# Performance work log

Measured on AMD Instinct MI355X. Metric: run time of the kernel, lower is better.

## Reference

```python
import jax, jax.numpy as jnp
import numpy as np

B, N, D_IN, D_OUT = 2, 2048, 2048, 2048
H, G = 16, 4            # num_heads, n_kv_groups
HD = D_OUT // H         # head_dim = 128
REP = H // G            # query heads per kv head = 4


def setup_inputs() -> dict:
    key = jax.random.key(0)
    ks = jax.random.split(key, 6)
    s = lambda fan_in: 1.0 / np.sqrt(fan_in)
    return {
        "x": jax.random.normal(ks[0], (B, N, D_IN), jnp.float32),
        "Wq": jax.random.normal(ks[1], (D_IN, D_OUT), jnp.float32) * s(D_IN),
        "Wk": jax.random.normal(ks[2], (D_IN, G * HD), jnp.float32) * s(D_IN),
        "Wv": jax.random.normal(ks[3], (D_IN, G * HD), jnp.float32) * s(D_IN),
        "Wo": jax.random.normal(ks[4], (D_OUT, D_OUT), jnp.float32) * s(D_OUT),
        "bo": jnp.zeros((D_OUT,), jnp.float32),
    }


def reference(x, Wq, Wk, Wv, Wo, bo):
    b, n, _ = x.shape
    # projections
    q = (x @ Wq).reshape(b, n, G, REP, HD)   # query heads grouped: h = g*REP + r
    k = (x @ Wk).reshape(b, n, G, HD)
    v = (x @ Wv).reshape(b, n, G, HD)
    # grouped attention scores; KV broadcast over REP instead of repeat_kv
    scores = jnp.einsum('bqgrd,bkgd->bgrqk', q, k)  # [b,G,REP,N,N]
    causal = jnp.tril(jnp.ones((n, n), bool))       # allowed positions
    scores = jnp.where(causal, scores, -jnp.inf)
    w = jax.nn.softmax(scores / np.float32(np.sqrt(HD)), axis=-1)
    ctx = jnp.einsum('bgrqk,bkgd->bqgrd', w, v).reshape(b, n, D_OUT)
    return ctx @ Wo + bo
```

## Files before the change

### kernel.cpp

```cpp
#include <hip/hip_runtime.h>
#include <stdint.h>

typedef __attribute__((ext_vector_type(8))) __bf16 bf16x8;
typedef __attribute__((ext_vector_type(4))) float f32x4;
typedef __attribute__((ext_vector_type(4))) short short4v;

static constexpr int SEQ  = 2048;
static constexpr int DQKV = 3072;
static constexpr int HD   = 128;

__device__ __forceinline__ short f2bf(float f) {
  unsigned u = __builtin_bit_cast(unsigned, f);
  u += 0x7fffu + ((u >> 16) & 1u);
  return (short)(u >> 16);
}

__device__ __forceinline__ unsigned pack2(float a, float b) {
  return (unsigned)(unsigned short)f2bf(a) | ((unsigned)(unsigned short)f2bf(b) << 16);
}

__device__ __forceinline__ void gl_lds16(const void* g, void* l) {
  __builtin_amdgcn_global_load_lds(
      (const __attribute__((address_space(1))) void*)g,
      (__attribute__((address_space(3))) void*)l, 16, 0, 0);
}

__global__ __launch_bounds__(256) void cast_x_kernel(const float* __restrict__ x,
                                                     short* __restrict__ xb) {
  int i = blockIdx.x * 256 + threadIdx.x;
  float4 v = reinterpret_cast<const float4*>(x)[i];
  short4v o;
  o[0] = f2bf(v.x); o[1] = f2bf(v.y); o[2] = f2bf(v.z); o[3] = f2bf(v.w);
  *reinterpret_cast<short4v*>(xb + (size_t)i * 4) = o;
}

__global__ __launch_bounds__(256) void tcast_w_kernel(const float* __restrict__ in,
                                                      short* __restrict__ out,
                                                      int R, int C) {
  __shared__ float tile[32][33];
  int c0 = blockIdx.x * 32, r0 = blockIdx.y * 32;
  int tx = threadIdx.x, ty = threadIdx.y;
  for (int i = 0; i < 4; i++)
    tile[ty + i * 8][tx] = in[(size_t)(r0 + ty + i * 8) * C + c0 + tx];
  __syncthreads();
  for (int i = 0; i < 4; i++)
    out[(size_t)(c0 + ty + i * 8) * R + r0 + tx] = f2bf(tile[tx][ty + i * 8]);
}

__global__ __launch_bounds__(256) void transpose_v_kernel(const short* __restrict__ qkv,
                                                          short* __restrict__ vT) {
  __shared__ short tile[32][33];
  int n0 = blockIdx.x * 32, c0 = blockIdx.y * 32, b = blockIdx.z;
  int tx = threadIdx.x, ty = threadIdx.y;
  for (int i = 0; i < 4; i++)
    tile[ty + i * 8][tx] = qkv[(size_t)(b * SEQ + n0 + ty + i * 8) * DQKV + 2560 + c0 + tx];
  __syncthreads();
  for (int i = 0; i < 4; i++)
    vT[(size_t)(b * 512 + c0 + ty + i * 8) * SEQ + n0 + tx] = tile[tx][ty + i * 8];
}

template <int F32OUT>
__global__ __launch_bounds__(256)
void gemm_bt_kernel(const short* __restrict__ A, const short* __restrict__ BT,
                    void* __restrict__ Cout, const float* __restrict__ bias,
                    int M, int N, int K, int qcols, float qscale) {
  __shared__ __align__(16) short As[4096];
  __shared__ __align__(16) short Bs[4096];
  const int tid = threadIdx.x, lane = tid & 63, w = tid >> 6;
  const int l15 = lane & 15, quad = lane >> 4, q8 = quad * 8;
  const int row0 = blockIdx.y * 128, col0 = blockIdx.x * 128;
  const int wm = (w >> 1) * 64, wn = (w & 1) * 64;
  f32x4 acc[4][4] = {};
  const short* ga0 = A  + (size_t)(row0 + w * 16 + (lane >> 2)) * K + (lane & 3) * 8;
  const short* gb0 = BT + (size_t)(col0 + w * 16 + (lane >> 2)) * K + (lane & 3) * 8;
  for (int kt = 0; kt < K; kt += 32) {
    gl_lds16(ga0 + kt,                   As + w * 512);
    gl_lds16(ga0 + (size_t)64 * K + kt,  As + 2048 + w * 512);
    gl_lds16(gb0 + kt,                   Bs + w * 512);
    gl_lds16(gb0 + (size_t)64 * K + kt,  Bs + 2048 + w * 512);
    __syncthreads();
    bf16x8 af[4], bfr[4];
    for (int i = 0; i < 4; i++)
      af[i] = *reinterpret_cast<const bf16x8*>(As + (wm + i * 16 + l15) * 32 + q8);
    for (int j = 0; j < 4; j++)
      bfr[j] = *reinterpret_cast<const bf16x8*>(Bs + (wn + j * 16 + l15) * 32 + q8);
    for (int i = 0; i < 4; i++)
      for (int j = 0; j < 4; j++)
        acc[i][j] = __builtin_amdgcn_mfma_f32_16x16x32_bf16(af[i], bfr[j], acc[i][j], 0, 0, 0);
    __syncthreads();
  }
  if (F32OUT) {
    float* C = (float*)Cout;
    for (int j = 0; j < 4; j++) {
      int col = col0 + wn + j * 16 + l15;
      float bv = bias[col];
      for (int i = 0; i < 4; i++)
        for (int r = 0; r < 4; r++)
          C[(size_t)(row0 + wm + i * 16 + quad * 4 + r) * N + col] = acc[i][j][r] + bv;
    }
  } else {
    short* C = (short*)Cout;
    for (int j = 0; j < 4; j++) {
      int col = col0 + wn + j * 16 + l15;
      float sc = (col < qcols) ? qscale : 1.0f;
      for (int i = 0; i < 4; i++)
        for (int r = 0; r < 4; r++)
          C[(size_t)(row0 + wm + i * 16 + quad * 4 + r) * N + col] = f2bf(acc[i][j][r] * sc);
    }
  }
}

__global__ __launch_bounds__(256)
void attn_kernel(const short* __restrict__ qkv, const short* __restrict__ vT,
                 short* __restrict__ ctx) {
  __shared__ __align__(16) short Ks[8192];
  __shared__ __align__(16) short Vs[8192];
  __shared__ __align__(16) short Ps[4608];
  const int tid = threadIdx.x, lane = tid & 63, w = tid >> 6;
  const int l15 = lane & 15, quad = lane >> 4, q8 = quad * 8;
  const int idx = blockIdx.x;
  const int qt = 31 - (idx >> 5);
  const int h = (idx >> 1) & 15, b = idx & 1, g = h >> 2;

  bf16x8 qf[4];
  {
    const short* gq = qkv + (size_t)(b * SEQ + qt * 64 + w * 16 + l15) * DQKV + h * HD + q8;
    for (int ds = 0; ds < 4; ds++)
      qf[ds] = *reinterpret_cast<const bf16x8*>(gq + ds * 32);
  }
  bf16x8 ones;
  for (int i = 0; i < 8; i++) ones[i] = __builtin_bit_cast(__bf16, (short)0x3F80);

  f32x4 acco[8] = {};
  f32x4 accl = {};

  for (int kt = 0; kt <= qt; kt++) {
    __syncthreads();
    {
      const short* gk = qkv + (size_t)(b * SEQ + kt * 64 + w * 16 + (lane >> 2)) * DQKV +
                        2048 + g * HD + (lane & 3) * 8;
      for (int ks = 0; ks < 4; ks++)
        gl_lds16(gk + ks * 32, Ks + ks * 2048 + w * 512);
      for (int c = 0; c < 2; c++)
        for (int ih = 0; ih < 2; ih++)
          gl_lds16(vT + (size_t)(b * 512 + g * HD + ih * 64 + w * 16 + (lane >> 2)) * SEQ +
                       kt * 64 + c * 32 + (lane & 3) * 8,
                   Vs + c * 4096 + ih * 2048 + w * 512);
    }
    __syncthreads();

    f32x4 accs[4] = {};
    for (int ds = 0; ds < 4; ds++)
      for (int j = 0; j < 4; j++) {
        bf16x8 kf = *reinterpret_cast<const bf16x8*>(Ks + ds * 2048 + (j * 16 + l15) * 32 + q8);
        accs[j] = __builtin_amdgcn_mfma_f32_16x16x32_bf16(kf, qf[ds], accs[j], 0, 0, 0);
      }

    if (kt == qt) {
      const int q = w * 16 + l15;
      for (int j = 0; j < 4; j++)
        for (int r = 0; r < 4; r++)
          if (j * 16 + quad * 4 + r > q) accs[j][r] = -1e38f;
    }

    for (int j = 0; j < 4; j++) {
      float p0 = exp2f(accs[j][0]), p1 = exp2f(accs[j][1]);
      float p2 = exp2f(accs[j][2]), p3 = exp2f(accs[j][3]);
      unsigned u0 = __builtin_bit_cast(unsigned, p0), u1 = __builtin_bit_cast(unsigned, p1);
      unsigned u2 = __builtin_bit_cast(unsigned, p2), u3 = __builtin_bit_cast(unsigned, p3);
      uint2 dd = make_uint2((u0 >> 16) | (u1 & 0xffff0000u),
                            (u2 >> 16) | (u3 & 0xffff0000u));
      *reinterpret_cast<uint2*>(Ps + w * 1152 + l15 * 72 + j * 16 + quad * 4) = dd;
    }
    asm volatile("s_waitcnt lgkmcnt(0)" ::: "memory");

    for (int c = 0; c < 2; c++) {
      bf16x8 pf = *reinterpret_cast<const bf16x8*>(Ps + w * 1152 + l15 * 72 + c * 32 + q8);
      accl = __builtin_amdgcn_mfma_f32_16x16x32_bf16(ones, pf, accl, 0, 0, 0);
      for (int nt = 0; nt < 8; nt++) {
        bf16x8 vf = *reinterpret_cast<const bf16x8*>(Vs + c * 4096 + (nt * 16 + l15) * 32 + q8);
        acco[nt] = __builtin_amdgcn_mfma_f32_16x16x32_bf16(vf, pf, acco[nt], 0, 0, 0);
      }
    }
  }

  const float invl = 1.f / accl[0];
  const size_t row = (size_t)(b * SEQ + qt * 64 + w * 16 + l15);
  for (int nt = 0; nt < 8; nt++) {
    uint2 dd = make_uint2(pack2(acco[nt][0] * invl, acco[nt][1] * invl),
                          pack2(acco[nt][2] * invl, acco[nt][3] * invl));
    *reinterpret_cast<uint2*>(ctx + row * 2048 + h * HD + nt * 16 + quad * 4) = dd;
  }
}

extern "C" void kernel_launch(void* const* d_in, const int* in_sizes, int n_in,
                              void* d_out, int out_size, void* d_ws, size_t ws_size,
                              hipStream_t stream) {
  const float* x  = (const float*)d_in[0];
  const float* Wq = (const float*)d_in[1];
  const float* Wk = (const float*)d_in[2];
  const float* Wv = (const float*)d_in[3];
  const float* Wo = (const float*)d_in[4];
  const float* bo = (const float*)d_in[5];
  float* out = (float*)d_out;

  const float sc2 = 0.08838834764831845f * 1.4426950408889634f;

  short* xb    = (short*)d_ws;
  short* WqkvT = xb    + (size_t)4096 * 2048;
  short* WoT   = WqkvT + (size_t)3072 * 2048;
  short* qkv   = WoT   + (size_t)2048 * 2048;
  short* vT    = qkv   + (size_t)4096 * 3072;
  short* ctx   = vT    + (size_t)1024 * 2048;

  cast_x_kernel<<<dim3(8192), dim3(256), 0, stream>>>(x, xb);
  tcast_w_kernel<<<dim3(64, 64), dim3(32, 8), 0, stream>>>(Wq, WqkvT, 2048, 2048);
  tcast_w_kernel<<<dim3(16, 64), dim3(32, 8), 0, stream>>>(Wk, WqkvT + (size_t)2048 * 2048, 2048, 512);
  tcast_w_kernel<<<dim3(16, 64), dim3(32, 8), 0, stream>>>(Wv, WqkvT + (size_t)2560 * 2048, 2048, 512);
  tcast_w_kernel<<<dim3(64, 64), dim3(32, 8), 0, stream>>>(Wo, WoT, 2048, 2048);

  gemm_bt_kernel<0><<<dim3(24, 32), dim3(256), 0, stream>>>(xb, WqkvT, qkv, nullptr,
                                                            4096, 3072, 2048, 2048, sc2);
  transpose_v_kernel<<<dim3(64, 16, 2), dim3(32, 8), 0, stream>>>(qkv, vT);
  attn_kernel<<<dim3(1024), dim3(256), 0, stream>>>(qkv, vT, ctx);
  gemm_bt_kernel<1><<<dim3(16, 32), dim3(256), 0, stream>>>(ctx, WoT, out, bo,
                                                            4096, 2048, 2048, 0, 1.0f);
}
```

Before: 325.3 us.

## Fuse prep kernels, fold V transpose into QKV GEMM, double-buffer attention K/V

Merges the x cast and four weight transpose-casts into a single launch, and writes the transposed V directly from the QKV GEMM epilogue, removing the separate transpose kernel. GEMM blocks use a swizzled 1D grid to group tiles for cache locality. The attention kernel double-buffers K/V tiles in LDS so the next tile's loads overlap compute, at the cost of doubled LDS use per block.

```diff
diff --git a/kernel.cpp b/kernel.cpp
--- a/kernel.cpp
+++ b/kernel.cpp
@@ -25,21 +25,30 @@
       (__attribute__((address_space(3))) void*)l, 16, 0, 0);
 }
 
-__global__ __launch_bounds__(256) void cast_x_kernel(const float* __restrict__ x,
-                                                     short* __restrict__ xb) {
-  int i = blockIdx.x * 256 + threadIdx.x;
-  float4 v = reinterpret_cast<const float4*>(x)[i];
-  short4v o;
-  o[0] = f2bf(v.x); o[1] = f2bf(v.y); o[2] = f2bf(v.z); o[3] = f2bf(v.w);
-  *reinterpret_cast<short4v*>(xb + (size_t)i * 4) = o;
-}
-
-__global__ __launch_bounds__(256) void tcast_w_kernel(const float* __restrict__ in,
-                                                      short* __restrict__ out,
-                                                      int R, int C) {
+__global__ __launch_bounds__(256)
+void prep_kernel(const float* __restrict__ x, const float* __restrict__ Wq,
+                 const float* __restrict__ Wk, const float* __restrict__ Wv,
+                 const float* __restrict__ Wo,
+                 short* __restrict__ xb, short* __restrict__ WqkvT,
+                 short* __restrict__ WoT) {
+  int blk = blockIdx.x, tid = threadIdx.x;
+  if (blk < 8192) {
+    int i = blk * 256 + tid;
+    float4 v = reinterpret_cast<const float4*>(x)[i];
+    short4v o;
+    o[0] = f2bf(v.x); o[1] = f2bf(v.y); o[2] = f2bf(v.z); o[3] = f2bf(v.w);
+    *reinterpret_cast<short4v*>(xb + (size_t)i * 4) = o;
+    return;
+  }
+  blk -= 8192;
   __shared__ float tile[32][33];
-  int c0 = blockIdx.x * 32, r0 = blockIdx.y * 32;
-  int tx = threadIdx.x, ty = threadIdx.y;
+  const float* in; short* out; int C, bx, by;
+  if (blk < 4096)      { in = Wq; out = WqkvT;                     C = 2048; bx = blk & 63; by = blk >> 6; }
+  else if (blk < 5120) { int t = blk - 4096; in = Wk; out = WqkvT + (size_t)2048 * 2048; C = 512; bx = t & 15; by = t >> 4; }
+  else if (blk < 6144) { int t = blk - 5120; in = Wv; out = WqkvT + (size_t)2560 * 2048; C = 512; bx = t & 15; by = t >> 4; }
+  else                 { int t = blk - 6144; in = Wo; out = WoT;   C = 2048; bx = t & 63; by = t >> 6; }
+  const int R = 2048;
+  int c0 = bx * 32, r0 = by * 32, tx = tid & 31, ty = tid >> 5;
   for (int i = 0; i < 4; i++)
     tile[ty + i * 8][tx] = in[(size_t)(r0 + ty + i * 8) * C + c0 + tx];
   __syncthreads();
@@ -47,28 +56,19 @@
     out[(size_t)(c0 + ty + i * 8) * R + r0 + tx] = f2bf(tile[tx][ty + i * 8]);
 }
 
-__global__ __launch_bounds__(256) void transpose_v_kernel(const short* __restrict__ qkv,
-                                                          short* __restrict__ vT) {
-  __shared__ short tile[32][33];
-  int n0 = blockIdx.x * 32, c0 = blockIdx.y * 32, b = blockIdx.z;
-  int tx = threadIdx.x, ty = threadIdx.y;
-  for (int i = 0; i < 4; i++)
-    tile[ty + i * 8][tx] = qkv[(size_t)(b * SEQ + n0 + ty + i * 8) * DQKV + 2560 + c0 + tx];
-  __syncthreads();
-  for (int i = 0; i < 4; i++)
-    vT[(size_t)(b * 512 + c0 + ty + i * 8) * SEQ + n0 + tx] = tile[tx][ty + i * 8];
-}
-
-template <int F32OUT>
-__global__ __launch_bounds__(256)
-void gemm_bt_kernel(const short* __restrict__ A, const short* __restrict__ BT,
-                    void* __restrict__ Cout, const float* __restrict__ bias,
-                    int M, int N, int K, int qcols, float qscale) {
+template <int MODE>
+__device__ __forceinline__
+void gemm_body(const short* __restrict__ A, const short* __restrict__ BT,
+               void* __restrict__ Cout, const float* __restrict__ bias,
+               short* __restrict__ vTout, int N, int K, int GX, float qscale) {
   __shared__ __align__(16) short As[4096];
   __shared__ __align__(16) short Bs[4096];
   const int tid = threadIdx.x, lane = tid & 63, w = tid >> 6;
   const int l15 = lane & 15, quad = lane >> 4, q8 = quad * 8;
-  const int row0 = blockIdx.y * 128, col0 = blockIdx.x * 128;
+  const int bid = blockIdx.x, stripe = GX >> 3;
+  const int bx = (bid & 7) * stripe + ((bid >> 3) % stripe);
+  const int by = (bid >> 3) / stripe;
+  const int row0 = by * 128, col0 = bx * 128;
   const int wm = (w >> 1) * 64, wn = (w & 1) * 64;
   f32x4 acc[4][4] = {};
   const short* ga0 = A  + (size_t)(row0 + w * 16 + (lane >> 2)) * K + (lane & 3) * 8;
@@ -89,7 +89,7 @@
         acc[i][j] = __builtin_amdgcn_mfma_f32_16x16x32_bf16(af[i], bfr[j], acc[i][j], 0, 0, 0);
     __syncthreads();
   }
-  if (F32OUT) {
+  if (MODE == 1) {
     float* C = (float*)Cout;
     for (int j = 0; j < 4; j++) {
       int col = col0 + wn + j * 16 + l15;
@@ -102,19 +102,46 @@
     short* C = (short*)Cout;
     for (int j = 0; j < 4; j++) {
       int col = col0 + wn + j * 16 + l15;
-      float sc = (col < qcols) ? qscale : 1.0f;
+      float sc = (col < 2048) ? qscale : 1.0f;
       for (int i = 0; i < 4; i++)
         for (int r = 0; r < 4; r++)
           C[(size_t)(row0 + wm + i * 16 + quad * 4 + r) * N + col] = f2bf(acc[i][j][r] * sc);
     }
+    if (col0 >= 2560) {
+      for (int j = 0; j < 4; j++) {
+        int vc = col0 + wn + j * 16 + l15 - 2560;
+        for (int i = 0; i < 4; i++) {
+          int rowg = row0 + wm + i * 16 + quad * 4;
+          int b = rowg >> 11, n = rowg & 2047;
+          uint2 dd = make_uint2(
+              (unsigned)(unsigned short)f2bf(acc[i][j][0]) |
+                  ((unsigned)(unsigned short)f2bf(acc[i][j][1]) << 16),
+              (unsigned)(unsigned short)f2bf(acc[i][j][2]) |
+                  ((unsigned)(unsigned short)f2bf(acc[i][j][3]) << 16));
+          *reinterpret_cast<uint2*>(vTout + (size_t)(b * 512 + vc) * 2048 + n) = dd;
+        }
+      }
+    }
   }
 }
 
 __global__ __launch_bounds__(256)
+void qkv_gemm_kernel(const short* __restrict__ A, const short* __restrict__ BT,
+                     short* __restrict__ C, short* __restrict__ vT, float qscale) {
+  gemm_body<0>(A, BT, C, nullptr, vT, 3072, 2048, 24, qscale);
+}
+
+__global__ __launch_bounds__(256)
+void out_gemm_kernel(const short* __restrict__ A, const short* __restrict__ BT,
+                     float* __restrict__ C, const float* __restrict__ bias) {
+  gemm_body<1>(A, BT, C, bias, nullptr, 2048, 2048, 16, 1.0f);
+}
+
+__global__ __launch_bounds__(256, 2)
 void attn_kernel(const short* __restrict__ qkv, const short* __restrict__ vT,
                  short* __restrict__ ctx) {
-  __shared__ __align__(16) short Ks[8192];
-  __shared__ __align__(16) short Vs[8192];
+  __shared__ __align__(16) short Ks[16384];
+  __shared__ __align__(16) short Vs[16384];
   __shared__ __align__(16) short Ps[4608];
   const int tid = threadIdx.x, lane = tid & 63, w = tid >> 6;
   const int l15 = lane & 15, quad = lane >> 4, q8 = quad * 8;
@@ -134,25 +161,31 @@
   f32x4 acco[8] = {};
   f32x4 accl = {};
 
+  auto stage = [&](int buf, int kt) {
+    const short* gk = qkv + (size_t)(b * SEQ + kt * 64 + w * 16 + (lane >> 2)) * DQKV +
+                      2048 + g * HD + (lane & 3) * 8;
+    for (int ks = 0; ks < 4; ks++)
+      gl_lds16(gk + ks * 32, Ks + buf * 8192 + ks * 2048 + w * 512);
+    for (int c = 0; c < 2; c++)
+      for (int ih = 0; ih < 2; ih++)
+        gl_lds16(vT + (size_t)(b * 512 + g * HD + ih * 64 + w * 16 + (lane >> 2)) * SEQ +
+                     kt * 64 + c * 32 + (lane & 3) * 8,
+                 Vs + buf * 8192 + c * 4096 + ih * 2048 + w * 512);
+  };
+
+  stage(0, 0);
   for (int kt = 0; kt <= qt; kt++) {
+    const int cur = kt & 1;
     __syncthreads();
-    {
-      const short* gk = qkv + (size_t)(b * SEQ + kt * 64 + w * 16 + (lane >> 2)) * DQKV +
-                        2048 + g * HD + (lane & 3) * 8;
-      for (int ks = 0; ks < 4; ks++)
-        gl_lds16(gk + ks * 32, Ks + ks * 2048 + w * 512);
-      for (int c = 0; c < 2; c++)
-        for (int ih = 0; ih < 2; ih++)
-          gl_lds16(vT + (size_t)(b * 512 + g * HD + ih * 64 + w * 16 + (lane >> 2)) * SEQ +
-                       kt * 64 + c * 32 + (lane & 3) * 8,
-                   Vs + c * 4096 + ih * 2048 + w * 512);
-    }
-    __syncthreads();
+    if (kt < qt) stage(cur ^ 1, kt + 1);
+
+    const short* Kb = Ks + cur * 8192;
+    const short* Vb = Vs + cur * 8192;
 
     f32x4 accs[4] = {};
     for (int ds = 0; ds < 4; ds++)
       for (int j = 0; j < 4; j++) {
-        bf16x8 kf = *reinterpret_cast<const bf16x8*>(Ks + ds * 2048 + (j * 16 + l15) * 32 + q8);
+        bf16x8 kf = *reinterpret_cast<const bf16x8*>(Kb + ds * 2048 + (j * 16 + l15) * 32 + q8);
         accs[j] = __builtin_amdgcn_mfma_f32_16x16x32_bf16(kf, qf[ds], accs[j], 0, 0, 0);
       }
 
@@ -178,7 +211,7 @@
       bf16x8 pf = *reinterpret_cast<const bf16x8*>(Ps + w * 1152 + l15 * 72 + c * 32 + q8);
       accl = __builtin_amdgcn_mfma_f32_16x16x32_bf16(ones, pf, accl, 0, 0, 0);
       for (int nt = 0; nt < 8; nt++) {
-        bf16x8 vf = *reinterpret_cast<const bf16x8*>(Vs + c * 4096 + (nt * 16 + l15) * 32 + q8);
+        bf16x8 vf = *reinterpret_cast<const bf16x8*>(Vb + c * 4096 + (nt * 16 + l15) * 32 + q8);
         acco[nt] = __builtin_amdgcn_mfma_f32_16x16x32_bf16(vf, pf, acco[nt], 0, 0, 0);
       }
     }
@@ -213,16 +246,8 @@
   short* vT    = qkv   + (size_t)4096 * 3072;
   short* ctx   = vT    + (size_t)1024 * 2048;
 
-  cast_x_kernel<<<dim3(8192), dim3(256), 0, stream>>>(x, xb);
-  tcast_w_kernel<<<dim3(64, 64), dim3(32, 8), 0, stream>>>(Wq, WqkvT, 2048, 2048);
-  tcast_w_kernel<<<dim3(16, 64), dim3(32, 8), 0, stream>>>(Wk, WqkvT + (size_t)2048 * 2048, 2048, 512);
-  tcast_w_kernel<<<dim3(16, 64), dim3(32, 8), 0, stream>>>(Wv, WqkvT + (size_t)2560 * 2048, 2048, 512);
-  tcast_w_kernel<<<dim3(64, 64), dim3(32, 8), 0, stream>>>(Wo, WoT, 2048, 2048);
-
-  gemm_bt_kernel<0><<<dim3(24, 32), dim3(256), 0, stream>>>(xb, WqkvT, qkv, nullptr,
-                                                            4096, 3072, 2048, 2048, sc2);
-  transpose_v_kernel<<<dim3(64, 16, 2), dim3(32, 8), 0, stream>>>(qkv, vT);
+  prep_kernel<<<dim3(18432), dim3(256), 0, stream>>>(x, Wq, Wk, Wv, Wo, xb, WqkvT, WoT);
+  qkv_gemm_kernel<<<dim3(768), dim3(256), 0, stream>>>(xb, WqkvT, qkv, vT, sc2);
   attn_kernel<<<dim3(1024), dim3(256), 0, stream>>>(qkv, vT, ctx);
-  gemm_bt_kernel<1><<<dim3(16, 32), dim3(256), 0, stream>>>(ctx, WoT, out, bo,
-                                                            4096, 2048, 2048, 0, 1.0f);
-}
+  out_gemm_kernel<<<dim3(512), dim3(256), 0, stream>>>(ctx, WoT, out, bo);
+}
```

Result: faster. 314.3 us (-3.4%).
